# Optimization experiments

Hardware: AMD Instinct MI355X
Metric: run time of the kernel (lower is better)

## Reference

```python
import jax, jax.numpy as jnp
import numpy as np

B, S, D = 2, 2048, 1024
E, K = 8, 2
CAP_FACTOR = 1.25
HID = 4 * D


def _capacity(num_tokens: int) -> int:
    import math
    cap = math.floor(K * CAP_FACTOR * num_tokens / E)
    cap += cap % 2
    return max(int(cap), 2)


def setup_inputs() -> dict:
    key = jax.random.key(0)
    k1, k2, k3, k4 = jax.random.split(key, 4)
    x = jax.random.normal(k1, (B, S, D), dtype=jnp.float32)
    w_gate = jax.random.normal(k2, (D, E), dtype=jnp.float32) * 0.02
    w_fc = jax.random.normal(k3, (E, D, HID), dtype=jnp.float32) * 0.02
    w_proj = jax.random.normal(k4, (E, HID, D), dtype=jnp.float32) * 0.02
    return {"x": x, "w_gate": w_gate, "w_fc": w_fc, "w_proj": w_proj}


def _moe_forward(x, w_gate, w_fc, w_proj):
    b, s, d = x.shape
    T = b * s
    cap = _capacity(T)
    xf = x.astype(jnp.float32).reshape(T, d)

    # --- Router (fp32, eval mode: no noise) ---
    logits = xf @ w_gate                                   # [T, E]
    top_v, top_i = jax.lax.top_k(logits, K)                # [T, K]
    NEG = jnp.float32(-1e30)
    masked = jnp.full_like(logits, NEG)
    masked = masked.at[jnp.arange(T)[:, None], top_i].set(top_v)
    probs = jax.nn.softmax(masked, axis=-1)                # [T, E], zero off top-k

    # --- Capacity assignment: cumsum over (k-major, token) flattened order ---
    oh = jax.nn.one_hot(top_i, E, dtype=jnp.int32)         # [T, K, E]
    oh = jnp.transpose(oh, (1, 0, 2))                      # [K, T, E]
    rank = jnp.cumsum(oh.reshape(K * T, E), axis=0).reshape(K, T, E) - 1
    within = (oh > 0) & (rank < cap)                       # [K, T, E]
    rank_sel = jnp.sum(jnp.where(within, rank, 0), axis=-1)  # [K, T]
    kept = jnp.any(within, axis=-1)                        # [K, T]

    p = jnp.take_along_axis(probs, top_i, axis=-1).T       # [K, T]
    w = jnp.where(kept, p, 0.0)                            # combine weights

    e_idx = top_i.T                                        # [K, T]
    t_idx = jnp.broadcast_to(jnp.arange(T)[None, :], (K, T))

    # expert_weights[t, e, c] (sparse scatter == torch one-hot combine)
    expert_weights = jnp.zeros((T, E, cap), jnp.float32)
    expert_weights = expert_weights.at[t_idx.ravel(), e_idx.ravel(), rank_sel.ravel()].add(w.ravel())

    # dispatch: expert_batches[e, c, :] = x of token routed to (e, c)
    disp = jnp.where(kept, 1.0, 0.0).ravel()[:, None]      # [K*T, 1]
    expert_batches = jnp.zeros((E, cap, d), jnp.float32)
    expert_batches = expert_batches.at[e_idx.ravel(), rank_sel.ravel()].add(disp * xf[t_idx.ravel()])

    # --- Expert MLPs (batched GEMMs, exact GELU, no bias, eval dropout) ---
    h = jnp.einsum('ecd,edh->ech', expert_batches, w_fc)
    h = jax.nn.gelu(h, approximate=False)
    expert_out = jnp.einsum('ech,ehd->ecd', h, w_proj)      # [E, cap, d]

    # --- Combine: gather expert outputs back to tokens weighted by router prob ---
    gathered = expert_out[e_idx.ravel(), rank_sel.ravel()].reshape(K, T, d)
    out_flat = jnp.sum(w[:, :, None] * gathered, axis=0)    # [T, d]
    output = out_flat.reshape(b, s, d)

    # --- Load balance loss (Switch) ---
    probs_full = jax.nn.softmax(logits, axis=-1)
    prob_per_expert = jnp.mean(probs_full, axis=0)          # [E]
    tokens_per_expert = jax.lax.stop_gradient(
        jnp.sum((expert_weights > 0).astype(jnp.float32), axis=(0, 2)) / (T * K)
    )
    lb_loss = E * jnp.sum(prob_per_expert * tokens_per_expert)

    # --- Router z-loss ---
    z_loss = jnp.mean(jax.nn.logsumexp(logits, axis=-1) ** 2)
    return output, lb_loss, z_loss


def reference(x, w_gate, w_fc, w_proj):
    return _moe_forward(x, w_gate, w_fc, w_proj)
```

## Files before the change

kernel.cpp:

```cpp
#include <hip/hip_runtime.h>
#include <hip/hip_bf16.h>
#include <cstdint>
#include <cstddef>

#define T_TOK 4096
#define D_DIM 1024
#define E_EXP 8
#define KSEL 2
#define CAP 1280
#define HID_DIM 4096

typedef __attribute__((ext_vector_type(8))) __bf16 bf16x8;
typedef __attribute__((ext_vector_type(8))) unsigned short ushort8;
typedef __attribute__((ext_vector_type(4))) float floatx4;

__device__ __forceinline__ unsigned short f2bf(float f) {
  unsigned int u = __builtin_bit_cast(unsigned int, f);
  u = (u + 0x7FFFu + ((u >> 16) & 1u)) >> 16;
  return (unsigned short)u;
}
__device__ __forceinline__ float bf2f(unsigned short h) {
  unsigned int u = ((unsigned int)h) << 16;
  return __builtin_bit_cast(float, u);
}

__device__ __forceinline__ void async16(const unsigned short* g, unsigned short* l) {
  __builtin_amdgcn_global_load_lds(
      (const __attribute__((address_space(1))) unsigned int*)g,
      (__attribute__((address_space(3))) unsigned int*)l, 16, 0, 0);
}

__global__ void router_kernel(const float* __restrict__ x, const float* __restrict__ wg,
                              int* __restrict__ top1, int* __restrict__ top2,
                              float* __restrict__ p0, float* __restrict__ p1,
                              float* __restrict__ lps_part, float* __restrict__ lz_part) {
  __shared__ float lps[E_EXP];
  __shared__ float lz;
  if (threadIdx.x < E_EXP) lps[threadIdx.x] = 0.f;
  if (threadIdx.x == 0) lz = 0.f;
  __syncthreads();
  int wave = threadIdx.x >> 6;
  int lane = threadIdx.x & 63;
  int t = blockIdx.x * 4 + wave;
  const float4* xr = (const float4*)(x + (size_t)t * D_DIM);
  float acc[E_EXP];
#pragma unroll
  for (int e = 0; e < E_EXP; ++e) acc[e] = 0.f;
#pragma unroll
  for (int j = 0; j < D_DIM / 256; ++j) {
    int i4 = lane + 64 * j;
    float4 xv = xr[i4];
    const float4* wr = (const float4*)(wg + (size_t)i4 * 4 * E_EXP);
    float4 w0 = wr[0], w1 = wr[1];
    float4 w2 = wr[2], w3 = wr[3];
    float4 w4 = wr[4], w5 = wr[5];
    float4 w6 = wr[6], w7 = wr[7];
    acc[0] += xv.x * w0.x + xv.y * w2.x + xv.z * w4.x + xv.w * w6.x;
    acc[1] += xv.x * w0.y + xv.y * w2.y + xv.z * w4.y + xv.w * w6.y;
    acc[2] += xv.x * w0.z + xv.y * w2.z + xv.z * w4.z + xv.w * w6.z;
    acc[3] += xv.x * w0.w + xv.y * w2.w + xv.z * w4.w + xv.w * w6.w;
    acc[4] += xv.x * w1.x + xv.y * w3.x + xv.z * w5.x + xv.w * w7.x;
    acc[5] += xv.x * w1.y + xv.y * w3.y + xv.z * w5.y + xv.w * w7.y;
    acc[6] += xv.x * w1.z + xv.y * w3.z + xv.z * w5.z + xv.w * w7.z;
    acc[7] += xv.x * w1.w + xv.y * w3.w + xv.z * w5.w + xv.w * w7.w;
  }
#pragma unroll
  for (int e = 0; e < E_EXP; ++e) {
#pragma unroll
    for (int s = 32; s > 0; s >>= 1) acc[e] += __shfl_xor(acc[e], s);
  }
  if (lane == 0) {
    int i1 = 0; float v1 = acc[0];
    for (int e = 1; e < E_EXP; ++e) if (acc[e] > v1) { v1 = acc[e]; i1 = e; }
    int i2 = -1; float v2 = -1e30f;
    for (int e = 0; e < E_EXP; ++e) if (e != i1 && acc[e] > v2) { v2 = acc[e]; i2 = e; }
    top1[t] = i1; top2[t] = i2;
    float dexp = expf(v2 - v1);
    p0[t] = 1.f / (1.f + dexp);
    p1[t] = dexp / (1.f + dexp);
    float pe[E_EXP]; float ssum = 0.f;
    for (int e = 0; e < E_EXP; ++e) { pe[e] = expf(acc[e] - v1); ssum += pe[e]; }
    float lse = logf(ssum) + v1;
    atomicAdd(&lz, lse * lse);
    float inv = 1.f / ssum;
    for (int e = 0; e < E_EXP; ++e) atomicAdd(&lps[e], pe[e] * inv);
  }
  __syncthreads();
  if (threadIdx.x < E_EXP) lps_part[(size_t)blockIdx.x * E_EXP + threadIdx.x] = lps[threadIdx.x];
  if (threadIdx.x == 0) lz_part[blockIdx.x] = lz;
}

__global__ void scan_kernel(const int* __restrict__ top1, const int* __restrict__ top2,
                            const float* __restrict__ lps_part, const float* __restrict__ lz_part,
                            int* __restrict__ rank0, int* __restrict__ rank1,
                            int* __restrict__ slot_token, int* __restrict__ cntk,
                            float* __restrict__ probsum, float* __restrict__ zsum) {
  __shared__ int sc[256][E_EXP];
  __shared__ float red[4][E_EXP + 1];
  int c = threadIdx.x;

  {
    float myz = 0.f;
    float myp[E_EXP];
#pragma unroll
    for (int e = 0; e < E_EXP; ++e) myp[e] = 0.f;
    for (int i = c; i < T_TOK / 4; i += 256) {
      myz += lz_part[i];
#pragma unroll
      for (int e = 0; e < E_EXP; ++e) myp[e] += lps_part[(size_t)i * E_EXP + e];
    }
#pragma unroll
    for (int s = 32; s > 0; s >>= 1) {
      myz += __shfl_xor(myz, s);
#pragma unroll
      for (int e = 0; e < E_EXP; ++e) myp[e] += __shfl_xor(myp[e], s);
    }
    int wv = c >> 6, ln = c & 63;
    if (ln == 0) {
      red[wv][E_EXP] = myz;
      for (int e = 0; e < E_EXP; ++e) red[wv][e] = myp[e];
    }
    __syncthreads();
    if (c == 0) {
      float z = red[0][E_EXP] + red[1][E_EXP] + red[2][E_EXP] + red[3][E_EXP];
      zsum[0] = z;
      for (int e = 0; e < E_EXP; ++e)
        probsum[e] = red[0][e] + red[1][e] + red[2][e] + red[3][e];
    }
  }

  int e0l[16], e1l[16];
  int c0[E_EXP], c1[E_EXP];
#pragma unroll
  for (int e = 0; e < E_EXP; ++e) { c0[e] = 0; c1[e] = 0; }
#pragma unroll
  for (int j = 0; j < 16; ++j) {
    int t = c * 16 + j;
    int a = top1[t]; int b = top2[t];
    e0l[j] = a; e1l[j] = b;
    c0[a]++; c1[b]++;
  }
  for (int e = 0; e < E_EXP; ++e) sc[c][e] = c0[e];
  __syncthreads();
  for (int s = 1; s < 256; s <<= 1) {
    int tmp[E_EXP];
    if (c >= s) { for (int e = 0; e < E_EXP; ++e) tmp[e] = sc[c - s][e]; }
    __syncthreads();
    if (c >= s) { for (int e = 0; e < E_EXP; ++e) sc[c][e] += tmp[e]; }
    __syncthreads();
  }
  int off0[E_EXP], tot0[E_EXP];
  for (int e = 0; e < E_EXP; ++e) {
    off0[e] = (c > 0) ? sc[c - 1][e] : 0;
    tot0[e] = sc[255][e];
  }
  __syncthreads();
  for (int e = 0; e < E_EXP; ++e) sc[c][e] = c1[e];
  __syncthreads();
  for (int s = 1; s < 256; s <<= 1) {
    int tmp[E_EXP];
    if (c >= s) { for (int e = 0; e < E_EXP; ++e) tmp[e] = sc[c - s][e]; }
    __syncthreads();
    if (c >= s) { for (int e = 0; e < E_EXP; ++e) sc[c][e] += tmp[e]; }
    __syncthreads();
  }
  int off1[E_EXP], tot1[E_EXP];
  for (int e = 0; e < E_EXP; ++e) {
    off1[e] = (c > 0) ? sc[c - 1][e] : 0;
    tot1[e] = sc[255][e];
  }
  int run[E_EXP];
  for (int e = 0; e < E_EXP; ++e) run[e] = off0[e];
#pragma unroll
  for (int j = 0; j < 16; ++j) {
    int t = c * 16 + j;
    int e = e0l[j];
    int r = run[e]++;
    if (r < CAP) { rank0[t] = r; slot_token[e * CAP + r] = t; } else rank0[t] = -1;
  }
  for (int e = 0; e < E_EXP; ++e) run[e] = tot0[e] + off1[e];
#pragma unroll
  for (int j = 0; j < 16; ++j) {
    int t = c * 16 + j;
    int e = e1l[j];
    int r = run[e]++;
    if (r < CAP) { rank1[t] = r; slot_token[e * CAP + r] = t; } else rank1[t] = -1;
  }
  for (int e = 0; e < E_EXP; ++e) {
    int tot = tot0[e] + tot1[e];
    int cnt = tot < CAP ? tot : CAP;
    for (int r = cnt + c; r < CAP; r += 256) slot_token[e * CAP + r] = -1;
    if (c == 0) cntk[e] = cnt;
  }
}

__global__ void dispatch_kernel(const float* __restrict__ x, const int* __restrict__ slot_token,
                                unsigned short* __restrict__ batch) {
  int slot = blockIdx.x;
  int t = slot_token[slot];
  int d = threadIdx.x * 4;
  ushort4 o;
  if (t >= 0) {
    float4 v = *(const float4*)(x + (size_t)t * D_DIM + d);
    o.x = f2bf(v.x); o.y = f2bf(v.y); o.z = f2bf(v.z); o.w = f2bf(v.w);
  } else {
    o.x = 0; o.y = 0; o.z = 0; o.w = 0;
  }
  *(ushort4*)(batch + (size_t)slot * D_DIM + d) = o;
}

__global__ __launch_bounds__(256) void transpose_convert(const float* __restrict__ in,
                                                         unsigned short* __restrict__ out,
                                                         int R, int C) {
  __shared__ float tile[64][65];
  int b = blockIdx.z;
  int c0 = blockIdx.x * 64;
  int r0 = blockIdx.y * 64;
  const float* ip = in + (size_t)b * R * C;
  unsigned short* op = out + (size_t)b * R * C;
  int tid = threadIdx.x;
  int rr = tid >> 4;
  int cc = (tid & 15) * 4;
#pragma unroll
  for (int it = 0; it < 4; ++it) {
    int r = rr + it * 16;
    float4 v = *(const float4*)(ip + (size_t)(r0 + r) * C + c0 + cc);
    tile[r][cc] = v.x; tile[r][cc + 1] = v.y; tile[r][cc + 2] = v.z; tile[r][cc + 3] = v.w;
  }
  __syncthreads();
  int c = tid >> 2;
  int rq = (tid & 3) * 16;
  unsigned short vals[16];
#pragma unroll
  for (int j = 0; j < 16; ++j) vals[j] = f2bf(tile[rq + j][c]);
  unsigned short* dst = op + (size_t)(c0 + c) * R + r0 + rq;
  *(ushort8*)dst = *(ushort8*)&vals[0];
  *(ushort8*)(dst + 8) = *(ushort8*)&vals[8];
}

template <int KD, int NN, int NG_TILES, bool GELU>
__global__ __launch_bounds__(256) void gemm_alds(const unsigned short* __restrict__ A,
                                                 const unsigned short* __restrict__ BT,
                                                 unsigned short* __restrict__ Cd,
                                                 const int* __restrict__ cntk) {
  constexpr int MT = CAP / 128;
  constexpr int GRP = MT * NG_TILES;
  int bid = blockIdx.x;
  int e = bid & 7;
  int slot = bid >> 3;
  int ng = slot / GRP;
  int rem = slot - ng * GRP;
  int mm = rem / NG_TILES;
  int nw = rem - mm * NG_TILES;
  int m0 = mm * 128;
  int n0 = (ng * NG_TILES + nw) * 128;
  if (m0 >= cntk[e]) return;
  const unsigned short* Ae = A + (size_t)e * CAP * KD;
  const unsigned short* Be = BT + (size_t)e * NN * KD;
  unsigned short* Ce = Cd + (size_t)e * CAP * NN;
  __shared__ unsigned short As[128 * 32];
  __shared__ unsigned short Bs[128 * 32];
  int tid = threadIdx.x;
  int lane = tid & 63;
  int wv = tid >> 6;
  int wm = (wv & 1) * 64;
  int wn = (wv >> 1) * 64;
  int mrow = lane & 15;
  int kqb = lane >> 4;
  int sx = (mrow >> 1) & 3;
  int kb = (kqb ^ sx) * 8;
  floatx4 acc[4][4];
#pragma unroll
  for (int i = 0; i < 4; ++i)
#pragma unroll
    for (int j = 0; j < 4; ++j) {
      floatx4 z = {0.f, 0.f, 0.f, 0.f};
      acc[i][j] = z;
    }
  for (int k0 = 0; k0 < KD; k0 += 32) {
#pragma unroll
    for (int i = 0; i < 2; ++i) {
      int chw = i * 256 + wv * 64;
      int ch = chw + lane;
      int r = ch >> 2;
      int cbs = (ch & 3) ^ ((r >> 1) & 3);
      async16(&Ae[(size_t)(m0 + r) * KD + k0 + cbs * 8], &As[chw * 8]);
      async16(&Be[(size_t)(n0 + r) * KD + k0 + cbs * 8], &Bs[chw * 8]);
    }
    __syncthreads();
    bf16x8 af[4], bfr[4];
#pragma unroll
    for (int mt = 0; mt < 4; ++mt)
      af[mt] = *(const bf16x8*)(&As[(wm + mt * 16 + mrow) * 32 + kb]);
#pragma unroll
    for (int nt = 0; nt < 4; ++nt)
      bfr[nt] = *(const bf16x8*)(&Bs[(wn + nt * 16 + mrow) * 32 + kb]);
#pragma unroll
    for (int mt = 0; mt < 4; ++mt)
#pragma unroll
      for (int nt = 0; nt < 4; ++nt)
        acc[mt][nt] = __builtin_amdgcn_mfma_f32_16x16x32_bf16(af[mt], bfr[nt], acc[mt][nt], 0, 0, 0);
    __syncthreads();
  }
  int crow = (lane >> 4) * 4;
  int ccol = lane & 15;
#pragma unroll
  for (int mt = 0; mt < 4; ++mt)
#pragma unroll
    for (int nt = 0; nt < 4; ++nt)
#pragma unroll
      for (int r = 0; r < 4; ++r) {
        float v = acc[mt][nt][r];
        if (GELU) v = 0.5f * v * (1.f + erff(v * 0.70710678118654752f));
        Ce[(size_t)(m0 + wm + mt * 16 + crow + r) * NN + (n0 + wn + nt * 16 + ccol)] = f2bf(v);
      }
}

__global__ void combine_kernel(const unsigned short* __restrict__ EO,
                               const int* __restrict__ top1, const int* __restrict__ top2,
                               const float* __restrict__ p0, const float* __restrict__ p1,
                               const int* __restrict__ rank0, const int* __restrict__ rank1,
                               const float* __restrict__ probsum, const float* __restrict__ zsum,
                               const int* __restrict__ cntk, float* __restrict__ out) {
  int t = blockIdx.x;
  int d = threadIdx.x * 4;
  float a0 = 0.f, a1 = 0.f, a2 = 0.f, a3 = 0.f;
  int r0 = rank0[t];
  if (r0 >= 0) {
    float w = p0[t];
    ushort4 v = *(const ushort4*)(EO + ((size_t)top1[t] * CAP + r0) * D_DIM + d);
    a0 += w * bf2f(v.x); a1 += w * bf2f(v.y); a2 += w * bf2f(v.z); a3 += w * bf2f(v.w);
  }
  int r1 = rank1[t];
  if (r1 >= 0) {
    float w = p1[t];
    ushort4 v = *(const ushort4*)(EO + ((size_t)top2[t] * CAP + r1) * D_DIM + d);
    a0 += w * bf2f(v.x); a1 += w * bf2f(v.y); a2 += w * bf2f(v.z); a3 += w * bf2f(v.w);
  }
  float4 o; o.x = a0; o.y = a1; o.z = a2; o.w = a3;
  *(float4*)(out + (size_t)t * D_DIM + d) = o;
  if (t == 0 && threadIdx.x == 0) {
    float lb = 0.f;
    for (int e = 0; e < E_EXP; ++e)
      lb += (probsum[e] / (float)T_TOK) * ((float)cntk[e] / (float)(T_TOK * KSEL));
    out[(size_t)T_TOK * D_DIM] = lb * (float)E_EXP;
    out[(size_t)T_TOK * D_DIM + 1] = zsum[0] / (float)T_TOK;
  }
}

extern "C" void kernel_launch(void* const* d_in, const int* in_sizes, int n_in,
                              void* d_out, int out_size, void* d_ws, size_t ws_size,
                              hipStream_t stream) {
  const float* x = (const float*)d_in[0];
  const float* w_gate = (const float*)d_in[1];
  const float* w_fc = (const float*)d_in[2];
  const float* w_proj = (const float*)d_in[3];
  float* out = (float*)d_out;
  char* ws = (char*)d_ws;

  float* probsum = (float*)(ws + 0);
  float* zsum    = (float*)(ws + 32);
  int*   cntk    = (int*)(ws + 64);
  int*   top1    = (int*)(ws + 4096);
  int*   top2    = (int*)(ws + 20480);
  float* p0      = (float*)(ws + 36864);
  float* p1      = (float*)(ws + 53248);
  int*   rank0   = (int*)(ws + 69632);
  int*   rank1   = (int*)(ws + 86016);
  int*   slot    = (int*)(ws + 102400);
  float* lz_part = (float*)(ws + 143360);
  float* lps_part= (float*)(ws + 147456);
  unsigned short* batch = (unsigned short*)(ws + 262144);
  unsigned short* H     = (unsigned short*)(ws + 262144 + 20971520);
  unsigned short* EO    = (unsigned short*)(ws + 262144 + 20971520 + 83886080);
  unsigned short* W     = (unsigned short*)(ws + 262144 + 20971520 + 83886080 + 20971520);

  router_kernel<<<T_TOK / 4, 256, 0, stream>>>(x, w_gate, top1, top2, p0, p1, lps_part, lz_part);
  scan_kernel<<<1, 256, 0, stream>>>(top1, top2, lps_part, lz_part,
                                     rank0, rank1, slot, cntk, probsum, zsum);
  dispatch_kernel<<<E_EXP * CAP, 256, 0, stream>>>(x, slot, batch);

  transpose_convert<<<dim3(HID_DIM / 64, D_DIM / 64, E_EXP), 256, 0, stream>>>(w_fc, W, D_DIM, HID_DIM);
  gemm_alds<D_DIM, HID_DIM, 4, true><<<8 * (HID_DIM / 128 / 4) * (CAP / 128) * 4, 256, 0, stream>>>(batch, W, H, cntk);

  transpose_convert<<<dim3(D_DIM / 64, HID_DIM / 64, E_EXP), 256, 0, stream>>>(w_proj, W, HID_DIM, D_DIM);
  gemm_alds<HID_DIM, D_DIM, 2, false><<<8 * (D_DIM / 128 / 2) * (CAP / 128) * 2, 256, 0, stream>>>(H, W, EO, cntk);

  combine_kernel<<<T_TOK, 256, 0, stream>>>(EO, top1, top2, p0, p1, rank0, rank1,
                                            probsum, zsum, cntk, out);
}
```

Before: 572.9 us.

## Fuse fp32 weight transpose-convert into expert GEMM B-tile loads

After: 617.1 us. +7.7%, slower.

```diff
diff --git a/kernel.cpp b/kernel.cpp
--- a/kernel.cpp
+++ b/kernel.cpp
@@ -13,6 +13,7 @@
 typedef __attribute__((ext_vector_type(8))) __bf16 bf16x8;
 typedef __attribute__((ext_vector_type(8))) unsigned short ushort8;
 typedef __attribute__((ext_vector_type(4))) float floatx4;
+typedef __attribute__((ext_vector_type(4))) unsigned int uintx4;
 
 __device__ __forceinline__ unsigned short f2bf(float f) {
   unsigned int u = __builtin_bit_cast(unsigned int, f);
@@ -209,40 +210,11 @@
   *(ushort4*)(batch + (size_t)slot * D_DIM + d) = o;
 }
 
-__global__ __launch_bounds__(256) void transpose_convert(const float* __restrict__ in,
-                                                         unsigned short* __restrict__ out,
-                                                         int R, int C) {
-  __shared__ float tile[64][65];
-  int b = blockIdx.z;
-  int c0 = blockIdx.x * 64;
-  int r0 = blockIdx.y * 64;
-  const float* ip = in + (size_t)b * R * C;
-  unsigned short* op = out + (size_t)b * R * C;
-  int tid = threadIdx.x;
-  int rr = tid >> 4;
-  int cc = (tid & 15) * 4;
-#pragma unroll
-  for (int it = 0; it < 4; ++it) {
-    int r = rr + it * 16;
-    float4 v = *(const float4*)(ip + (size_t)(r0 + r) * C + c0 + cc);
-    tile[r][cc] = v.x; tile[r][cc + 1] = v.y; tile[r][cc + 2] = v.z; tile[r][cc + 3] = v.w;
-  }
-  __syncthreads();
-  int c = tid >> 2;
-  int rq = (tid & 3) * 16;
-  unsigned short vals[16];
-#pragma unroll
-  for (int j = 0; j < 16; ++j) vals[j] = f2bf(tile[rq + j][c]);
-  unsigned short* dst = op + (size_t)(c0 + c) * R + r0 + rq;
-  *(ushort8*)dst = *(ushort8*)&vals[0];
-  *(ushort8*)(dst + 8) = *(ushort8*)&vals[8];
-}
-
 template <int KD, int NN, int NG_TILES, bool GELU>
-__global__ __launch_bounds__(256) void gemm_alds(const unsigned short* __restrict__ A,
-                                                 const unsigned short* __restrict__ BT,
-                                                 unsigned short* __restrict__ Cd,
-                                                 const int* __restrict__ cntk) {
+__global__ __launch_bounds__(256) void gemm_fused(const unsigned short* __restrict__ A,
+                                                  const float* __restrict__ Wnat,
+                                                  unsigned short* __restrict__ Cd,
+                                                  const int* __restrict__ cntk) {
   constexpr int MT = CAP / 128;
   constexpr int GRP = MT * NG_TILES;
   int bid = blockIdx.x;
@@ -256,7 +228,7 @@
   int n0 = (ng * NG_TILES + nw) * 128;
   if (m0 >= cntk[e]) return;
   const unsigned short* Ae = A + (size_t)e * CAP * KD;
-  const unsigned short* Be = BT + (size_t)e * NN * KD;
+  const float* Be = Wnat + (size_t)e * KD * NN;
   unsigned short* Ce = Cd + (size_t)e * CAP * NN;
   __shared__ unsigned short As[128 * 32];
   __shared__ unsigned short Bs[128 * 32];
@@ -269,6 +241,14 @@
   int kqb = lane >> 4;
   int sx = (mrow >> 1) & 3;
   int kb = (kqb ^ sx) * 8;
+
+  const int nB = tid & 127;
+  const int cb0 = tid >> 7;
+  const int swB = (nB >> 1) & 3;
+  unsigned short* bdst0 = &Bs[(nB * 4 + (cb0 ^ swB)) * 8];
+  unsigned short* bdst1 = &Bs[(nB * 4 + ((cb0 + 2) ^ swB)) * 8];
+  const float* bsrc = Be + n0 + nB;
+
   floatx4 acc[4][4];
 #pragma unroll
   for (int i = 0; i < 4; ++i)
@@ -277,7 +257,29 @@
       floatx4 z = {0.f, 0.f, 0.f, 0.f};
       acc[i][j] = z;
     }
+
+  float bpre[16];
+  {
+    const float* p0 = bsrc + (size_t)(cb0 * 8) * NN;
+    const float* p1 = bsrc + (size_t)(cb0 * 8 + 16) * NN;
+#pragma unroll
+    for (int j = 0; j < 8; ++j) {
+      bpre[j]     = p0[(size_t)j * NN];
+      bpre[8 + j] = p1[(size_t)j * NN];
+    }
+  }
+
   for (int k0 = 0; k0 < KD; k0 += 32) {
+    {
+      uintx4 lo, hi;
+#pragma unroll
+      for (int jj = 0; jj < 4; ++jj) {
+        lo[jj] = (unsigned int)f2bf(bpre[2 * jj]) | ((unsigned int)f2bf(bpre[2 * jj + 1]) << 16);
+        hi[jj] = (unsigned int)f2bf(bpre[8 + 2 * jj]) | ((unsigned int)f2bf(bpre[8 + 2 * jj + 1]) << 16);
+      }
+      *(uintx4*)bdst0 = lo;
+      *(uintx4*)bdst1 = hi;
+    }
 #pragma unroll
     for (int i = 0; i < 2; ++i) {
       int chw = i * 256 + wv * 64;
@@ -285,7 +287,17 @@
       int r = ch >> 2;
       int cbs = (ch & 3) ^ ((r >> 1) & 3);
       async16(&Ae[(size_t)(m0 + r) * KD + k0 + cbs * 8], &As[chw * 8]);
-      async16(&Be[(size_t)(n0 + r) * KD + k0 + cbs * 8], &Bs[chw * 8]);
+    }
+    {
+      int kp = k0 + 32;
+      if (kp >= KD) kp = 0;
+      const float* p0 = bsrc + (size_t)(kp + cb0 * 8) * NN;
+      const float* p1 = bsrc + (size_t)(kp + cb0 * 8 + 16) * NN;
+#pragma unroll
+      for (int j = 0; j < 8; ++j) {
+        bpre[j]     = p0[(size_t)j * NN];
+        bpre[8 + j] = p1[(size_t)j * NN];
+      }
     }
     __syncthreads();
     bf16x8 af[4], bfr[4];
@@ -373,18 +385,17 @@
   unsigned short* batch = (unsigned short*)(ws + 262144);
   unsigned short* H     = (unsigned short*)(ws + 262144 + 20971520);
   unsigned short* EO    = (unsigned short*)(ws + 262144 + 20971520 + 83886080);
-  unsigned short* W     = (unsigned short*)(ws + 262144 + 20971520 + 83886080 + 20971520);
 
   router_kernel<<<T_TOK / 4, 256, 0, stream>>>(x, w_gate, top1, top2, p0, p1, lps_part, lz_part);
   scan_kernel<<<1, 256, 0, stream>>>(top1, top2, lps_part, lz_part,
                                      rank0, rank1, slot, cntk, probsum, zsum);
   dispatch_kernel<<<E_EXP * CAP, 256, 0, stream>>>(x, slot, batch);
 
-  transpose_convert<<<dim3(HID_DIM / 64, D_DIM / 64, E_EXP), 256, 0, stream>>>(w_fc, W, D_DIM, HID_DIM);
-  gemm_alds<D_DIM, HID_DIM, 4, true><<<8 * (HID_DIM / 128 / 4) * (CAP / 128) * 4, 256, 0, stream>>>(batch, W, H, cntk);
-
-  transpose_convert<<<dim3(D_DIM / 64, HID_DIM / 64, E_EXP), 256, 0, stream>>>(w_proj, W, HID_DIM, D_DIM);
-  gemm_alds<HID_DIM, D_DIM, 2, false><<<8 * (D_DIM / 128 / 2) * (CAP / 128) * 2, 256, 0, stream>>>(H, W, EO, cntk);
+  gemm_fused<D_DIM, HID_DIM, 4, true><<<8 * (HID_DIM / 128 / 4) * (CAP / 128) * 4, 256, 0, stream>>>(
+      batch, w_fc, H, cntk);
+
+  gemm_fused<HID_DIM, D_DIM, 2, false><<<8 * (D_DIM / 128 / 2) * (CAP / 128) * 2, 256, 0, stream>>>(
+      H, w_proj, EO, cntk);
 
   combine_kernel<<<T_TOK, 256, 0, stream>>>(EO, top1, top2, p0, p1, rank0, rank1,
                                             probsum, zsum, cntk, out);
```
